# Performance work log

Hardware: AMD Instinct MI355X
Metric: run time of the kernel (lower is better)

## Reference

```python
import jax, jax.numpy as jnp
import numpy as np

R_ITERS = 3
EPSILON = 1e-7


def squash(s, epsilon=EPSILON, axis=-1):
    # s: (..., dim); v = |s|^2/(1+|s|^2) * s/(|s|+eps)
    s_norm = jnp.linalg.norm(s, axis=axis, keepdims=True)
    sq = jnp.square(s_norm)
    return sq / (1.0 + sq) * (s / (s_norm + epsilon))


def setup_inputs() -> dict:
    key = jax.random.key(0)
    k1, k2 = jax.random.split(key)
    B, P, Dp = 128, 1152, 8     # batch, n_primary_caps, dim_primary_caps
    S, Ds = 32, 16              # n_secondary_caps, dim_secondary_caps
    x = jax.random.normal(k1, (B, P, Dp), dtype=jnp.float32)
    W = jax.random.normal(k2, (S, P, Ds, Dp), dtype=jnp.float32) * 0.05
    return {"x": x, "W": W}


def reference(x, W):
    # u_hat[b,s,p,j] = sum_i W[s,p,j,i] * x[b,p,i]  (replaces tf.map_fn+matmul)
    u_hat = jnp.einsum('spji,bpi->bspj', W, x)  # (B, S, P, Ds)
    B, S, P, Ds = u_hat.shape
    b_logits = jnp.zeros((B, S, P), dtype=u_hat.dtype)
    v = None
    for _ in range(R_ITERS):
        c = jax.nn.softmax(b_logits, axis=-1)                # (B, S, P)
        s_vec = jnp.einsum('bsp,bspj->bsj', c, u_hat)        # (B, S, Ds)
        v = squash(s_vec)                                    # (B, S, Ds)
        agreement = jnp.einsum('bsj,bspj->bsp', v, u_hat)    # (B, S, P)
        b_logits = b_logits + agreement
    return v  # (B, n_secondary_caps, dim_secondary_caps)
```

## Files before the change

kernel.cpp:

```cpp
#include <hip/hip_runtime.h>

#define P_SZ 1152
#define DP 8
#define DS 16
#define NTHR 512
#define NQ 128
#define PT 9
#define NW 8

__global__ __launch_bounds__(NTHR, 4)
void caps_routing9(const float* __restrict__ x, const float* __restrict__ W,
                   float* __restrict__ out) {
    __shared__ float red[2][NW][2][17];

    const int t    = threadIdx.x;
    const int lane = t & 63;
    const int jq   = t & 3;
    const int pq   = t >> 2;
    const int w    = t >> 6;
    const int bid  = blockIdx.x;
    const int s    = bid & 31;
    const int b0   = (bid >> 5) << 1;

    float uh0[PT][4], uh1[PT][4];

    const float* xb0 = x + (size_t)b0 * (P_SZ * DP);
    const float* xb1 = xb0 + P_SZ * DP;

    #pragma unroll
    for (int r = 0; r < PT; ++r) {
        const int p = (r << 7) + pq;
        const float* wp = W + (size_t)(s * P_SZ + p) * (DS * DP) + jq * DP;
        const float4 xa0 = *(const float4*)(xb0 + p * DP);
        const float4 xa1 = *(const float4*)(xb0 + p * DP + 4);
        const float4 xc0 = *(const float4*)(xb1 + p * DP);
        const float4 xc1 = *(const float4*)(xb1 + p * DP + 4);
        #pragma unroll
        for (int jj = 0; jj < 4; ++jj) {
            const float4 w0 = *(const float4*)(wp + jj * 32);
            const float4 w1 = *(const float4*)(wp + jj * 32 + 4);
            uh0[r][jj] = w0.x*xa0.x + w0.y*xa0.y + w0.z*xa0.z + w0.w*xa0.w
                       + w1.x*xa1.x + w1.y*xa1.y + w1.z*xa1.z + w1.w*xa1.w;
            uh1[r][jj] = w0.x*xc0.x + w0.y*xc0.y + w0.z*xc0.z + w0.w*xc0.w
                       + w1.x*xc1.x + w1.y*xc1.y + w1.z*xc1.z + w1.w*xc1.w;
        }
        __builtin_amdgcn_sched_barrier(0);
    }

    float sv0[4], sv1[4];
    #pragma unroll
    for (int jj = 0; jj < 4; ++jj) {
        float a = 0.f, c = 0.f;
        #pragma unroll
        for (int r = 0; r < PT; ++r) { a += uh0[r][jj]; c += uh1[r][jj]; }
        sv0[jj] = a; sv1[jj] = c;
    }
    #pragma unroll
    for (int off = 4; off < 64; off <<= 1) {
        #pragma unroll
        for (int jj = 0; jj < 4; ++jj) {
            sv0[jj] += __shfl_xor(sv0[jj], off);
            sv1[jj] += __shfl_xor(sv1[jj], off);
        }
    }
    if (lane < 4) {
        #pragma unroll
        for (int jj = 0; jj < 4; ++jj) {
            red[0][w][0][jq + 4*jj] = sv0[jj];
            red[0][w][1][jq + 4*jj] = sv1[jj];
        }
    }
    __syncthreads();
    #pragma unroll
    for (int jj = 0; jj < 4; ++jj) { sv0[jj] = 0.f; sv1[jj] = 0.f; }
    #pragma unroll
    for (int ww = 0; ww < NW; ++ww) {
        #pragma unroll
        for (int jj = 0; jj < 4; ++jj) {
            sv0[jj] += red[0][ww][0][jq + 4*jj];
            sv1[jj] += red[0][ww][1][jq + 4*jj];
        }
    }
    #pragma unroll
    for (int jj = 0; jj < 4; ++jj) { sv0[jj] *= (1.f / P_SZ); sv1[jj] *= (1.f / P_SZ); }

    float sq0 = sv0[0]*sv0[0] + sv0[1]*sv0[1] + sv0[2]*sv0[2] + sv0[3]*sv0[3];
    float sq1 = sv1[0]*sv1[0] + sv1[1]*sv1[1] + sv1[2]*sv1[2] + sv1[3]*sv1[3];
    sq0 += __shfl_xor(sq0, 1); sq0 += __shfl_xor(sq0, 2);
    sq1 += __shfl_xor(sq1, 1); sq1 += __shfl_xor(sq1, 2);
    float f0 = sq0 / (1.f + sq0) / (sqrtf(sq0) + 1e-7f);
    float f1 = sq1 / (1.f + sq1) / (sqrtf(sq1) + 1e-7f);
    float va0[4], va1[4];
    #pragma unroll
    for (int jj = 0; jj < 4; ++jj) { va0[jj] = f0 * sv0[jj]; va1[jj] = f1 * sv1[jj]; }

    #pragma unroll
    for (int it = 1; it < 3; ++it) {
        float es0 = 0.f, es1 = 0.f;
        #pragma unroll
        for (int jj = 0; jj < 4; ++jj) { sv0[jj] = 0.f; sv1[jj] = 0.f; }
        #pragma unroll
        for (int r = 0; r < PT; ++r) {
            float d0 = va0[0]*uh0[r][0] + va0[1]*uh0[r][1]
                     + va0[2]*uh0[r][2] + va0[3]*uh0[r][3];
            float d1 = va1[0]*uh1[r][0] + va1[1]*uh1[r][1]
                     + va1[2]*uh1[r][2] + va1[3]*uh1[r][3];
            d0 += __shfl_xor(d0, 1); d0 += __shfl_xor(d0, 2);
            d1 += __shfl_xor(d1, 1); d1 += __shfl_xor(d1, 2);
            const float e0 = __expf(d0);
            const float e1 = __expf(d1);
            es0 += e0; es1 += e1;
            #pragma unroll
            for (int jj = 0; jj < 4; ++jj) {
                sv0[jj] += e0 * uh0[r][jj];
                sv1[jj] += e1 * uh1[r][jj];
            }
        }
        #pragma unroll
        for (int off = 4; off < 64; off <<= 1) {
            es0 += __shfl_xor(es0, off);
            es1 += __shfl_xor(es1, off);
            #pragma unroll
            for (int jj = 0; jj < 4; ++jj) {
                sv0[jj] += __shfl_xor(sv0[jj], off);
                sv1[jj] += __shfl_xor(sv1[jj], off);
            }
        }
        const int buf = it & 1;
        if (lane < 4) {
            #pragma unroll
            for (int jj = 0; jj < 4; ++jj) {
                red[buf][w][0][jq + 4*jj] = sv0[jj];
                red[buf][w][1][jq + 4*jj] = sv1[jj];
            }
            if (lane == 0) { red[buf][w][0][16] = es0; red[buf][w][1][16] = es1; }
        }
        __syncthreads();
        es0 = 0.f; es1 = 0.f;
        #pragma unroll
        for (int jj = 0; jj < 4; ++jj) { sv0[jj] = 0.f; sv1[jj] = 0.f; }
        #pragma unroll
        for (int ww = 0; ww < NW; ++ww) {
            es0 += red[buf][ww][0][16];
            es1 += red[buf][ww][1][16];
            #pragma unroll
            for (int jj = 0; jj < 4; ++jj) {
                sv0[jj] += red[buf][ww][0][jq + 4*jj];
                sv1[jj] += red[buf][ww][1][jq + 4*jj];
            }
        }
        const float r0 = 1.f / es0, r1 = 1.f / es1;
        #pragma unroll
        for (int jj = 0; jj < 4; ++jj) { sv0[jj] *= r0; sv1[jj] *= r1; }

        sq0 = sv0[0]*sv0[0] + sv0[1]*sv0[1] + sv0[2]*sv0[2] + sv0[3]*sv0[3];
        sq1 = sv1[0]*sv1[0] + sv1[1]*sv1[1] + sv1[2]*sv1[2] + sv1[3]*sv1[3];
        sq0 += __shfl_xor(sq0, 1); sq0 += __shfl_xor(sq0, 2);
        sq1 += __shfl_xor(sq1, 1); sq1 += __shfl_xor(sq1, 2);
        f0 = sq0 / (1.f + sq0) / (sqrtf(sq0) + 1e-7f);
        f1 = sq1 / (1.f + sq1) / (sqrtf(sq1) + 1e-7f);

        if (it == 2) {
            if (t < 4) {
                #pragma unroll
                for (int jj = 0; jj < 4; ++jj)
                    out[(size_t)(b0 * 32 + s) * DS + jq + 4*jj] = f0 * sv0[jj];
            } else if (t < 8) {
                #pragma unroll
                for (int jj = 0; jj < 4; ++jj)
                    out[(size_t)((b0 + 1) * 32 + s) * DS + jq + 4*jj] = f1 * sv1[jj];
            }
        } else {
            #pragma unroll
            for (int jj = 0; jj < 4; ++jj) {
                va0[jj] += f0 * sv0[jj];
                va1[jj] += f1 * sv1[jj];
            }
        }
    }
}

extern "C" void kernel_launch(void* const* d_in, const int* in_sizes, int n_in,
                              void* d_out, int out_size, void* d_ws, size_t ws_size,
                              hipStream_t stream) {
    const float* x = (const float*)d_in[0];
    const float* W = (const float*)d_in[1];
    float* out = (float*)d_out;
    caps_routing9<<<dim3(32 * 64), dim3(NTHR), 0, stream>>>(x, W, out);
}
```

Measured before the change: 75.09 us.

## Remap blocks so each XCD shares W slices; use fast rcp/exp2 intrinsics

Block IDs are remapped so that, with round-robin dispatch across the 8 XCDs, all blocks for a given secondary capsule s land on the same XCD. Each XCD's L2 then serves repeated reads of that s's W slice instead of every XCD fetching all of W. The load loop now advances pointers incrementally instead of recomputing addresses. The exp, divide and sqrt calls become native amdgcn exp2/rcp/sqrt intrinsics with log2e folded into v, which trades a little accuracy for fewer instructions.

```diff
diff --git a/kernel.cpp b/kernel.cpp
--- a/kernel.cpp
+++ b/kernel.cpp
@@ -4,13 +4,12 @@
 #define DP 8
 #define DS 16
 #define NTHR 512
-#define NQ 128
 #define PT 9
 #define NW 8
 
 __global__ __launch_bounds__(NTHR, 4)
-void caps_routing9(const float* __restrict__ x, const float* __restrict__ W,
-                   float* __restrict__ out) {
+void caps_routing12(const float* __restrict__ x, const float* __restrict__ W,
+                    float* __restrict__ out) {
     __shared__ float red[2][NW][2][17];
 
     const int t    = threadIdx.x;
@@ -19,32 +18,37 @@
     const int pq   = t >> 2;
     const int w    = t >> 6;
     const int bid  = blockIdx.x;
-    const int s    = bid & 31;
-    const int b0   = (bid >> 5) << 1;
+    const int xcd  = bid & 7;
+    const int k    = bid >> 3;
+    const int s    = xcd + ((k >> 6) << 3);
+    const int b0   = (k & 63) << 1;
 
     float uh0[PT][4], uh1[PT][4];
 
-    const float* xb0 = x + (size_t)b0 * (P_SZ * DP);
-    const float* xb1 = xb0 + P_SZ * DP;
-
-    #pragma unroll
-    for (int r = 0; r < PT; ++r) {
-        const int p = (r << 7) + pq;
-        const float* wp = W + (size_t)(s * P_SZ + p) * (DS * DP) + jq * DP;
-        const float4 xa0 = *(const float4*)(xb0 + p * DP);
-        const float4 xa1 = *(const float4*)(xb0 + p * DP + 4);
-        const float4 xc0 = *(const float4*)(xb1 + p * DP);
-        const float4 xc1 = *(const float4*)(xb1 + p * DP + 4);
-        #pragma unroll
-        for (int jj = 0; jj < 4; ++jj) {
-            const float4 w0 = *(const float4*)(wp + jj * 32);
-            const float4 w1 = *(const float4*)(wp + jj * 32 + 4);
-            uh0[r][jj] = w0.x*xa0.x + w0.y*xa0.y + w0.z*xa0.z + w0.w*xa0.w
-                       + w1.x*xa1.x + w1.y*xa1.y + w1.z*xa1.z + w1.w*xa1.w;
-            uh1[r][jj] = w0.x*xc0.x + w0.y*xc0.y + w0.z*xc0.z + w0.w*xc0.w
-                       + w1.x*xc1.x + w1.y*xc1.y + w1.z*xc1.z + w1.w*xc1.w;
-        }
-        __builtin_amdgcn_sched_barrier(0);
+    {
+        const float* wp = W + ((size_t)s * P_SZ + pq) * (DS * DP) + jq * DP;
+        const float* xa = x + (size_t)b0 * (P_SZ * DP) + pq * DP;
+        const float* xc = xa + P_SZ * DP;
+        #pragma unroll
+        for (int r = 0; r < PT; ++r) {
+            const float4 xa0 = *(const float4*)(xa);
+            const float4 xa1 = *(const float4*)(xa + 4);
+            const float4 xc0 = *(const float4*)(xc);
+            const float4 xc1 = *(const float4*)(xc + 4);
+            #pragma unroll
+            for (int jj = 0; jj < 4; ++jj) {
+                const float4 w0 = *(const float4*)(wp + jj * 32);
+                const float4 w1 = *(const float4*)(wp + jj * 32 + 4);
+                uh0[r][jj] = w0.x*xa0.x + w0.y*xa0.y + w0.z*xa0.z + w0.w*xa0.w
+                           + w1.x*xa1.x + w1.y*xa1.y + w1.z*xa1.z + w1.w*xa1.w;
+                uh1[r][jj] = w0.x*xc0.x + w0.y*xc0.y + w0.z*xc0.z + w0.w*xc0.w
+                           + w1.x*xc1.x + w1.y*xc1.y + w1.z*xc1.z + w1.w*xc1.w;
+            }
+            wp += 128 * (DS * DP);
+            xa += 128 * DP;
+            xc += 128 * DP;
+            __builtin_amdgcn_sched_barrier(0);
+        }
     }
 
     float sv0[4], sv1[4];
@@ -88,27 +92,35 @@
     float sq1 = sv1[0]*sv1[0] + sv1[1]*sv1[1] + sv1[2]*sv1[2] + sv1[3]*sv1[3];
     sq0 += __shfl_xor(sq0, 1); sq0 += __shfl_xor(sq0, 2);
     sq1 += __shfl_xor(sq1, 1); sq1 += __shfl_xor(sq1, 2);
-    float f0 = sq0 / (1.f + sq0) / (sqrtf(sq0) + 1e-7f);
-    float f1 = sq1 / (1.f + sq1) / (sqrtf(sq1) + 1e-7f);
+    float f0 = sq0 * __builtin_amdgcn_rcpf(
+        (1.f + sq0) * (__builtin_amdgcn_sqrtf(sq0) + 1e-7f));
+    float f1 = sq1 * __builtin_amdgcn_rcpf(
+        (1.f + sq1) * (__builtin_amdgcn_sqrtf(sq1) + 1e-7f));
     float va0[4], va1[4];
     #pragma unroll
     for (int jj = 0; jj < 4; ++jj) { va0[jj] = f0 * sv0[jj]; va1[jj] = f1 * sv1[jj]; }
+
+    const float LOG2E = 1.4426950408889634f;
 
     #pragma unroll
     for (int it = 1; it < 3; ++it) {
         float es0 = 0.f, es1 = 0.f;
-        #pragma unroll
-        for (int jj = 0; jj < 4; ++jj) { sv0[jj] = 0.f; sv1[jj] = 0.f; }
+        float vas0[4], vas1[4];
+        #pragma unroll
+        for (int jj = 0; jj < 4; ++jj) {
+            vas0[jj] = va0[jj] * LOG2E; vas1[jj] = va1[jj] * LOG2E;
+            sv0[jj] = 0.f; sv1[jj] = 0.f;
+        }
         #pragma unroll
         for (int r = 0; r < PT; ++r) {
-            float d0 = va0[0]*uh0[r][0] + va0[1]*uh0[r][1]
-                     + va0[2]*uh0[r][2] + va0[3]*uh0[r][3];
-            float d1 = va1[0]*uh1[r][0] + va1[1]*uh1[r][1]
-                     + va1[2]*uh1[r][2] + va1[3]*uh1[r][3];
+            float d0 = vas0[0]*uh0[r][0] + vas0[1]*uh0[r][1]
+                     + vas0[2]*uh0[r][2] + vas0[3]*uh0[r][3];
+            float d1 = vas1[0]*uh1[r][0] + vas1[1]*uh1[r][1]
+                     + vas1[2]*uh1[r][2] + vas1[3]*uh1[r][3];
             d0 += __shfl_xor(d0, 1); d0 += __shfl_xor(d0, 2);
             d1 += __shfl_xor(d1, 1); d1 += __shfl_xor(d1, 2);
-            const float e0 = __expf(d0);
-            const float e1 = __expf(d1);
+            const float e0 = __builtin_amdgcn_exp2f(d0);
+            const float e1 = __builtin_amdgcn_exp2f(d1);
             es0 += e0; es1 += e1;
             #pragma unroll
             for (int jj = 0; jj < 4; ++jj) {
@@ -149,7 +161,8 @@
                 sv1[jj] += red[buf][ww][1][jq + 4*jj];
             }
         }
-        const float r0 = 1.f / es0, r1 = 1.f / es1;
+        const float r0 = __builtin_amdgcn_rcpf(es0);
+        const float r1 = __builtin_amdgcn_rcpf(es1);
         #pragma unroll
         for (int jj = 0; jj < 4; ++jj) { sv0[jj] *= r0; sv1[jj] *= r1; }
 
@@ -157,8 +170,10 @@
         sq1 = sv1[0]*sv1[0] + sv1[1]*sv1[1] + sv1[2]*sv1[2] + sv1[3]*sv1[3];
         sq0 += __shfl_xor(sq0, 1); sq0 += __shfl_xor(sq0, 2);
         sq1 += __shfl_xor(sq1, 1); sq1 += __shfl_xor(sq1, 2);
-        f0 = sq0 / (1.f + sq0) / (sqrtf(sq0) + 1e-7f);
-        f1 = sq1 / (1.f + sq1) / (sqrtf(sq1) + 1e-7f);
+        f0 = sq0 * __builtin_amdgcn_rcpf(
+            (1.f + sq0) * (__builtin_amdgcn_sqrtf(sq0) + 1e-7f));
+        f1 = sq1 * __builtin_amdgcn_rcpf(
+            (1.f + sq1) * (__builtin_amdgcn_sqrtf(sq1) + 1e-7f));
 
         if (it == 2) {
             if (t < 4) {
@@ -186,5 +201,5 @@
     const float* x = (const float*)d_in[0];
     const float* W = (const float*)d_in[1];
     float* out = (float*)d_out;
-    caps_routing9<<<dim3(32 * 64), dim3(NTHR), 0, stream>>>(x, W, out);
+    caps_routing12<<<dim3(32 * 64), dim3(NTHR), 0, stream>>>(x, W, out);
 }
```

New measurement: 92.52 us. +23.2%, slower.
